# Optimization experiments

Measured on AMD Instinct MI355X. Metric: run time of the kernel, lower is better.

## Reference

```python
import jax, jax.numpy as jnp
import numpy as np

B, N, CL = 128, 64, 64


def _lin_params(key, fan_in, fan_out):
    k1, k2 = jax.random.split(key)
    bound = 1.0 / np.sqrt(fan_in)
    w = jax.random.uniform(k1, (fan_in, fan_out), jnp.float32, -bound, bound)
    b = jax.random.uniform(k2, (fan_out,), jnp.float32, -bound, bound)
    return w, b


def setup_inputs() -> dict:
    key = jax.random.key(0)
    ks = jax.random.split(key, 12)
    cl = CL
    se_w1, se_b1 = _lin_params(ks[0], cl, cl)
    se_w2, se_b2 = _lin_params(ks[1], cl, cl)
    sd_w1, sd_b1 = _lin_params(ks[2], cl, 2 * cl)
    sd_w2, sd_b2 = _lin_params(ks[3], 2 * cl, 2 * cl)
    rc_w1, rc_b1 = _lin_params(ks[4], 2 * cl + 1, 2 * cl)
    rc_w2, rc_b2 = _lin_params(ks[5], 2 * cl, 2 * cl)
    rc_w3, rc_b3 = _lin_params(ks[6], 2 * cl, 2 * cl)
    an_w1, an_b1 = _lin_params(ks[7], 2 * cl + 1, cl)
    an_w2, an_b2 = _lin_params(ks[8], cl, 2 * cl)
    s = jax.random.normal(ks[9], (B, N, cl), jnp.float32)
    return dict(s=s,
                se_w1=se_w1, se_b1=se_b1, se_w2=se_w2, se_b2=se_b2,
                sd_w1=sd_w1, sd_b1=sd_b1, sd_w2=sd_w2, sd_b2=sd_b2,
                rc_w1=rc_w1, rc_b1=rc_b1, rc_w2=rc_w2, rc_b2=rc_b2,
                rc_w3=rc_w3, rc_b3=rc_b3,
                an_w1=an_w1, an_b1=an_b1, an_w2=an_w2, an_b2=an_b2)


def reference(s, se_w1, se_b1, se_w2, se_b2,
              sd_w1, sd_b1, sd_w2, sd_b2,
              rc_w1, rc_b1, rc_w2, rc_b2, rc_w3, rc_b3,
              an_w1, an_b1, an_w2, an_b2):
    relu = jax.nn.relu
    # state encoder: [B, N, cl]
    h = relu(relu(s @ se_w1 + se_b1) @ se_w2 + se_b2)
    Bn, Nn, cl = h.shape
    # all-pairs features [B, N, N, cl]
    a1 = jnp.broadcast_to(h[:, :, None, :], (Bn, Nn, Nn, cl))  # object_arg1
    a2 = jnp.broadcast_to(h[:, None, :, :], (Bn, Nn, Nn, cl))  # object_arg2
    dist = (a1[..., 0] - a2[..., 0]) ** 2 + (a1[..., 1] - a2[..., 1]) ** 2
    feat = jnp.concatenate([a1, a2, dist[..., None]], axis=-1)  # [B,N,N,2cl+1]
    rel = relu(relu(relu(feat @ rc_w1 + rc_b1) @ rc_w2 + rc_b2) @ rc_w3 + rc_b3)
    att = jax.nn.sigmoid(relu(feat @ an_w1 + an_b1) @ an_w2 + an_b2)
    rel_dyn = jnp.mean(rel * att, axis=2)  # [B, N, 2cl]
    self_dyn = relu(h @ sd_w1 + sd_b1) @ sd_w2 + sd_b2  # [B, N, 2cl]
    return jnp.mean(self_dyn + rel_dyn, axis=1)  # [B, 2cl]
```

## Files before the change

kernel.cpp:

```cpp
#include <hip/hip_runtime.h>
#include <math.h>

#define TPB 256

typedef unsigned short u16;
typedef __attribute__((ext_vector_type(8))) short bf16x8;
typedef __attribute__((ext_vector_type(4))) float f32x4;

#define BLOB_U16 524288
#define BASE_RC_F32 327680
#define BASE_AN_F32 1376256
#define WS_NEED_BASES ((size_t)(1376256 + 524288) * 4)
#define RC1F 0
#define AN1F 16384
#define AN2F 24576
#define RC2F 40960
#define RC3F 73728

__device__ __forceinline__ float b2f(u16 h) {
  return __uint_as_float(((unsigned)h) << 16);
}
__device__ __forceinline__ void split_bf16(float x, u16& hi, u16& lo) {
  unsigned u = __float_as_uint(x);
  hi = (u16)(u >> 16);
  float hif = __uint_as_float(u & 0xFFFF0000u);
  lo = (u16)(__float_as_uint(x - hif) >> 16);
}
__device__ __forceinline__ u16 f2bf_rne(float x) {
  unsigned u = __float_as_uint(x);
  return (u16)((u + 0x7FFFu + ((u >> 16) & 1u)) >> 16);
}
__device__ __forceinline__ unsigned pack_bf16_hu(float v0, float v1) {
  unsigned a = __float_as_uint(v0) + 0x8000u;
  unsigned b = __float_as_uint(v1) + 0x8000u;
  return __builtin_amdgcn_perm(b, a, 0x07060302u);
}

__device__ __forceinline__ void cp_lds(float* dst, const float* src, int nfloats, int tid) {
  const float4* s4 = (const float4*)src;
  float4* d4 = (float4*)dst;
  const int n4 = nfloats >> 2;
  for (int i = tid; i < n4; i += TPB) d4[i] = s4[i];
}
__device__ __forceinline__ void ld4(float r[4], const float* p) {
  float4 v = *(const float4*)p;
  r[0] = v.x; r[1] = v.y; r[2] = v.z; r[3] = v.w;
}
__device__ __forceinline__ void ld2(float r[2], const float* p) {
  float2 v = *(const float2*)p;
  r[0] = v.x; r[1] = v.y;
}

__global__ __launch_bounds__(TPB, 3) void enc_prep_kernel(
    const float* __restrict__ s_in,
    const float* __restrict__ se_w1, const float* __restrict__ se_b1,
    const float* __restrict__ se_w2, const float* __restrict__ se_b2,
    const float* __restrict__ sd_w1, const float* __restrict__ sd_b1,
    const float* __restrict__ sd_w2, const float* __restrict__ sd_b2,
    const float* __restrict__ rc_w1, const float* __restrict__ rc_b1,
    const float* __restrict__ rc_w2, const float* __restrict__ rc_w3,
    const float* __restrict__ an_w1, const float* __restrict__ an_b1,
    const float* __restrict__ an_w2,
    u16* __restrict__ hB, u16* __restrict__ blob,
    float* __restrict__ baseRcG, float* __restrict__ baseAnG, int do_bases,
    float* __restrict__ out) {
  if (blockIdx.x >= 256) {
    int idx = (int)(blockIdx.x - 256) * TPB + threadIdx.x;
    if (idx >= 53248) return;
    int r, base, OK, T; const float* W; int Wld, krow0, twoTerm;
    if (idx < 8192)       { r = idx;         base = RC1F; OK = 8192;  T = 8; W = rc_w1; Wld = 128; krow0 = 64; twoTerm = 1; }
    else if (idx < 12288) { r = idx - 8192;  base = AN1F; OK = 4096;  T = 4; W = an_w1; Wld = 64;  krow0 = 64; twoTerm = 1; }
    else if (idx < 20480) { r = idx - 12288; base = AN2F; OK = 8192;  T = 8; W = an_w2; Wld = 128; krow0 = 0;  twoTerm = 0; }
    else if (idx < 36864) { r = idx - 20480; base = RC2F; OK = 16384; T = 8; W = rc_w2; Wld = 128; krow0 = 0;  twoTerm = 0; }
    else                  { r = idx - 36864; base = RC3F; OK = 16384; T = 8; W = rc_w3; Wld = 128; krow0 = 0;  twoTerm = 0; }
    const int u = r & 7;
    const int lane = (r >> 3) & 63;
    const int ct = r >> 9;
    const int c = (T == 8) ? (ct >> 3) : (ct >> 2);
    const int tg = (T == 8) ? (ct & 7) : (ct & 3);
    const int o = tg * 16 + (lane & 15);
    const int k = c * 32 + (lane >> 4) * 8 + u;
    const float x = W[(krow0 + k) * Wld + o];
    if (twoTerm) {
      u16 hi, lo; split_bf16(x, hi, lo);
      blob[base + r] = hi;
      blob[base + OK + r] = lo;
    } else {
      blob[base + r] = f2bf_rne(x);
    }
    return;
  }

  __shared__ __align__(16) float sX[2048];
  __shared__ __align__(16) float sH1[2048];
  __shared__ __align__(16) float sT[4096];
  __shared__ __align__(16) float sW[4096];
  __shared__ float sb1[64], sb2[64], sdb1[128], sdb2[128], srb1[128], sab1[64];

  const int tid = threadIdx.x;
  const int lg = tid >> 5;
  const int og = tid & 31;
  const int b = blockIdx.x >> 1;
  const int row0 = b * 64 + (blockIdx.x & 1) * 32;
  const int n0 = lg * 4;

  cp_lds(sX, s_in + row0 * 64, 2048, tid);
  cp_lds(sW, se_w1, 4096, tid);
  if (tid < 64) { sb1[tid] = se_b1[tid]; sb2[tid] = se_b2[tid]; }
  else if (tid < 192) { const int o = tid - 64; sdb1[o] = sd_b1[o]; sdb2[o] = sd_b2[o]; }
  if (tid < 128) srb1[tid] = rc_b1[tid];
  else if (tid < 192) sab1[tid - 128] = an_b1[tid - 128];
  __syncthreads();

  float a2[4][2];
#pragma unroll
  for (int nn = 0; nn < 4; nn++) { a2[nn][0] = 0.f; a2[nn][1] = 0.f; }
  for (int kk = 0; kk < 64; kk += 4) {
    float xr[4][4], wr[4][2];
#pragma unroll
    for (int nn = 0; nn < 4; nn++) ld4(xr[nn], &sX[(n0 + nn) * 64 + kk]);
#pragma unroll
    for (int t = 0; t < 4; t++) ld2(wr[t], &sW[(kk + t) * 64 + og * 2]);
#pragma unroll
    for (int t = 0; t < 4; t++)
#pragma unroll
      for (int nn = 0; nn < 4; nn++) {
        a2[nn][0] = fmaf(xr[nn][t], wr[t][0], a2[nn][0]);
        a2[nn][1] = fmaf(xr[nn][t], wr[t][1], a2[nn][1]);
      }
  }
#pragma unroll
  for (int nn = 0; nn < 4; nn++) {
    float2 v;
    v.x = fmaxf(a2[nn][0] + sb1[og * 2 + 0], 0.f);
    v.y = fmaxf(a2[nn][1] + sb1[og * 2 + 1], 0.f);
    *(float2*)&sH1[(n0 + nn) * 64 + og * 2] = v;
  }
  __syncthreads();
  cp_lds(sW, se_w2, 4096, tid);
  __syncthreads();

#pragma unroll
  for (int nn = 0; nn < 4; nn++) { a2[nn][0] = 0.f; a2[nn][1] = 0.f; }
  for (int kk = 0; kk < 64; kk += 4) {
    float xr[4][4], wr[4][2];
#pragma unroll
    for (int nn = 0; nn < 4; nn++) ld4(xr[nn], &sH1[(n0 + nn) * 64 + kk]);
#pragma unroll
    for (int t = 0; t < 4; t++) ld2(wr[t], &sW[(kk + t) * 64 + og * 2]);
#pragma unroll
    for (int t = 0; t < 4; t++)
#pragma unroll
      for (int nn = 0; nn < 4; nn++) {
        a2[nn][0] = fmaf(xr[nn][t], wr[t][0], a2[nn][0]);
        a2[nn][1] = fmaf(xr[nn][t], wr[t][1], a2[nn][1]);
      }
  }
#pragma unroll
  for (int nn = 0; nn < 4; nn++) {
    float2 v;
    v.x = fmaxf(a2[nn][0] + sb2[og * 2 + 0], 0.f);
    v.y = fmaxf(a2[nn][1] + sb2[og * 2 + 1], 0.f);
    *(float2*)&sX[(n0 + nn) * 64 + og * 2] = v;
    const int off = (row0 + n0 + nn) * 64 + og * 2;
    *(ushort2*)&hB[off] = make_ushort2(f2bf_rne(v.x), f2bf_rne(v.y));
  }
  __syncthreads();

  float a4[4][4];
#pragma unroll
  for (int nn = 0; nn < 4; nn++)
#pragma unroll
    for (int oo = 0; oo < 4; oo++) a4[nn][oo] = 0.f;
  for (int c = 0; c < 2; c++) {
    cp_lds(sW, sd_w1 + c * 32 * 128, 4096, tid);
    __syncthreads();
    for (int kk = 0; kk < 32; kk += 4) {
      float xr[4][4], wr[4][4];
#pragma unroll
      for (int nn = 0; nn < 4; nn++) ld4(xr[nn], &sX[(n0 + nn) * 64 + c * 32 + kk]);
#pragma unroll
      for (int t = 0; t < 4; t++) ld4(wr[t], &sW[(kk + t) * 128 + og * 4]);
#pragma unroll
      for (int t = 0; t < 4; t++)
#pragma unroll
        for (int nn = 0; nn < 4; nn++)
#pragma unroll
          for (int oo = 0; oo < 4; oo++)
            a4[nn][oo] = fmaf(xr[nn][t], wr[t][oo], a4[nn][oo]);
    }
    __syncthreads();
  }
#pragma unroll
  for (int nn = 0; nn < 4; nn++) {
    float4 v;
    v.x = fmaxf(a4[nn][0] + sdb1[og * 4 + 0], 0.f);
    v.y = fmaxf(a4[nn][1] + sdb1[og * 4 + 1], 0.f);
    v.z = fmaxf(a4[nn][2] + sdb1[og * 4 + 2], 0.f);
    v.w = fmaxf(a4[nn][3] + sdb1[og * 4 + 3], 0.f);
    *(float4*)&sT[(n0 + nn) * 128 + og * 4] = v;
  }
  __syncthreads();

#pragma unroll
  for (int nn = 0; nn < 4; nn++)
#pragma unroll
    for (int oo = 0; oo < 4; oo++) a4[nn][oo] = 0.f;
  for (int c = 0; c < 4; c++) {
    cp_lds(sW, sd_w2 + c * 32 * 128, 4096, tid);
    __syncthreads();
    for (int kk = 0; kk < 32; kk += 4) {
      float xr[4][4], wr[4][4];
#pragma unroll
      for (int nn = 0; nn < 4; nn++) ld4(xr[nn], &sT[(n0 + nn) * 128 + c * 32 + kk]);
#pragma unroll
      for (int t = 0; t < 4; t++) ld4(wr[t], &sW[(kk + t) * 128 + og * 4]);
#pragma unroll
      for (int t = 0; t < 4; t++)
#pragma unroll
        for (int nn = 0; nn < 4; nn++)
#pragma unroll
          for (int oo = 0; oo < 4; oo++)
            a4[nn][oo] = fmaf(xr[nn][t], wr[t][oo], a4[nn][oo]);
    }
    __syncthreads();
  }
  float p[4];
#pragma unroll
  for (int oo = 0; oo < 4; oo++)
    p[oo] = a4[0][oo] + a4[1][oo] + a4[2][oo] + a4[3][oo] + 4.f * sdb2[og * 4 + oo];
  *(float4*)&sH1[lg * 128 + og * 4] = make_float4(p[0], p[1], p[2], p[3]);
  __syncthreads();
  if (tid < 128) {
    float ssum = 0.f;
#pragma unroll
    for (int g = 0; g < 8; g++) ssum += sH1[g * 128 + tid];
    atomicAdd(&out[b * 128 + tid], ssum * (1.0f / 64.0f));
  }

  if (do_bases) {
#pragma unroll
    for (int nn = 0; nn < 4; nn++)
#pragma unroll
      for (int oo = 0; oo < 4; oo++) a4[nn][oo] = 0.f;
    for (int c = 0; c < 2; c++) {
      __syncthreads();
      cp_lds(sW, rc_w1 + c * 32 * 128, 4096, tid);
      __syncthreads();
      for (int kk = 0; kk < 32; kk += 4) {
        float xr[4][4], wr[4][4];
#pragma unroll
        for (int nn = 0; nn < 4; nn++) ld4(xr[nn], &sX[(n0 + nn) * 64 + c * 32 + kk]);
#pragma unroll
        for (int t = 0; t < 4; t++) ld4(wr[t], &sW[(kk + t) * 128 + og * 4]);
#pragma unroll
        for (int t = 0; t < 4; t++)
#pragma unroll
          for (int nn = 0; nn < 4; nn++)
#pragma unroll
            for (int oo = 0; oo < 4; oo++)
              a4[nn][oo] = fmaf(xr[nn][t], wr[t][oo], a4[nn][oo]);
      }
    }
#pragma unroll
    for (int nn = 0; nn < 4; nn++) {
      float4 v;
      v.x = a4[nn][0] + srb1[og * 4 + 0];
      v.y = a4[nn][1] + srb1[og * 4 + 1];
      v.z = a4[nn][2] + srb1[og * 4 + 2];
      v.w = a4[nn][3] + srb1[og * 4 + 3];
      *(float4*)&baseRcG[(size_t)(row0 + n0 + nn) * 128 + og * 4] = v;
    }
    __syncthreads();
    cp_lds(sW, an_w1, 4096, tid);
    __syncthreads();
#pragma unroll
    for (int nn = 0; nn < 4; nn++) { a2[nn][0] = 0.f; a2[nn][1] = 0.f; }
    for (int kk = 0; kk < 64; kk += 4) {
      float xr[4][4], wr[4][2];
#pragma unroll
      for (int nn = 0; nn < 4; nn++) ld4(xr[nn], &sX[(n0 + nn) * 64 + kk]);
#pragma unroll
      for (int t = 0; t < 4; t++) ld2(wr[t], &sW[(kk + t) * 64 + og * 2]);
#pragma unroll
      for (int t = 0; t < 4; t++)
#pragma unroll
        for (int nn = 0; nn < 4; nn++) {
          a2[nn][0] = fmaf(xr[nn][t], wr[t][0], a2[nn][0]);
          a2[nn][1] = fmaf(xr[nn][t], wr[t][1], a2[nn][1]);
        }
    }
#pragma unroll
    for (int nn = 0; nn < 4; nn++) {
      float2 v;
      v.x = a2[nn][0] + sab1[og * 2 + 0];
      v.y = a2[nn][1] + sab1[og * 2 + 1];
      *(float2*)&baseAnG[(size_t)(row0 + n0 + nn) * 64 + og * 2] = v;
    }
  }
}

template<int MT, int NCHUNK, int RSG, int TILES>
__device__ __forceinline__ void run_layer2(f32x4 (&acc)[MT][4],
    const u16* __restrict__ blobL, int OK,
    const u16* __restrict__ sB, int tg0, int quad, int l15) {
  const int lane = quad * 16 + l15;
#pragma unroll
  for (int c = 0; c < NCHUNK; ++c) {
    bf16x8 Ah[MT], Al[MT];
#pragma unroll
    for (int t = 0; t < MT; ++t) {
      const u16* p = blobL + ((c * TILES + tg0 + t) * 64 + lane) * 8;
      Ah[t] = *(const bf16x8*)p;
      Al[t] = *(const bf16x8*)(p + OK);
    }
    const int slot = (4 * c + quad) ^ (l15 & 7);
    bf16x8 Bh[4];
#pragma unroll
    for (int s = 0; s < 4; ++s)
      Bh[s] = *(const bf16x8*)&sB[(16 * s + l15) * (RSG * 8) + slot * 8];
#pragma unroll
    for (int t = 0; t < MT; ++t)
#pragma unroll
      for (int s = 0; s < 4; ++s) {
        f32x4 a = acc[t][s];
        a = __builtin_amdgcn_mfma_f32_16x16x32_bf16(Ah[t], Bh[s], a, 0, 0, 0);
        a = __builtin_amdgcn_mfma_f32_16x16x32_bf16(Al[t], Bh[s], a, 0, 0, 0);
        acc[t][s] = a;
      }
  }
}

template<int MT, int NCHUNK, int RSG, int TILES>
__device__ __forceinline__ void run_layer1(f32x4 (&acc)[MT][4],
    const u16* __restrict__ blobL,
    const u16* __restrict__ sB, int tg0, int quad, int l15) {
  const int lane = quad * 16 + l15;
#pragma unroll
  for (int c = 0; c < NCHUNK; ++c) {
    bf16x8 Ah[MT];
#pragma unroll
    for (int t = 0; t < MT; ++t)
      Ah[t] = *(const bf16x8*)(blobL + ((c * TILES + tg0 + t) * 64 + lane) * 8);
    const int slot = (4 * c + quad) ^ (l15 & 7);
    bf16x8 Bh[4];
#pragma unroll
    for (int s = 0; s < 4; ++s)
      Bh[s] = *(const bf16x8*)&sB[(16 * s + l15) * (RSG * 8) + slot * 8];
#pragma unroll
    for (int t = 0; t < MT; ++t)
#pragma unroll
      for (int s = 0; s < 4; ++s)
        acc[t][s] = __builtin_amdgcn_mfma_f32_16x16x32_bf16(Ah[t], Bh[s], acc[t][s], 0, 0, 0);
  }
}

template<int MT, int RSG>
__device__ __forceinline__ void store_acts_pk(const f32x4 (&acc)[MT][4],
                                              u16* dst, int o0, int quad, int l15) {
#pragma unroll
  for (int t = 0; t < MT; ++t) {
    const int ob = o0 + 16 * t + quad * 4;
    const int slot = (ob >> 3) ^ (l15 & 7);
    const int e = ob & 7;
#pragma unroll
    for (int s = 0; s < 4; ++s) {
      const int j = 16 * s + l15;
      uint2 pk;
      pk.x = pack_bf16_hu(fmaxf(acc[t][s][0], 0.f), fmaxf(acc[t][s][1], 0.f));
      pk.y = pack_bf16_hu(fmaxf(acc[t][s][2], 0.f), fmaxf(acc[t][s][3], 0.f));
      *(uint2*)&dst[j * (RSG * 8) + slot * 8 + e] = pk;
    }
  }
}

__global__ __launch_bounds__(TPB, 4) void pair_mfma_kernel(
    const u16* __restrict__ hB, const u16* __restrict__ blob,
    const float* __restrict__ baseRcG, const float* __restrict__ baseAnG,
    int has_bases,
    const float* __restrict__ rc_w1, const float* __restrict__ rc_b1,
    const float* __restrict__ rc_b2, const float* __restrict__ rc_b3,
    const float* __restrict__ an_w1, const float* __restrict__ an_b1,
    const float* __restrict__ an_b2,
    float* __restrict__ out) {
  __shared__ __align__(16) u16 sAct[64 * 128];
  __shared__ __align__(16) u16 sAn[64 * 64];
  __shared__ float sHi[64], sDist[64];
  __shared__ float sBaseRc[128], sBaseAn[64], sW1d[128], sAnd[64];
  __shared__ float sB2[128], sB3[128], sAb2[128], sRed[128];

  const int tid = threadIdx.x;
  const int w = tid >> 6, lane = tid & 63;
  const int quad = lane >> 4, l15 = lane & 15;
  const int b = blockIdx.x >> 6, i = blockIdx.x & 63;
  const int o0 = w * 32;
  const int o0a = w * 16;

  {
    const float4* srcJ = (const float4*)(hB + b * 4096);
    for (int idx = tid; idx < 512; idx += TPB) {
      const int row = idx >> 3, g = idx & 7;
      *(float4*)&sAct[row * 128 + ((g ^ (row & 7)) * 8)] = srcJ[idx];
    }
  }
  if (has_bases) {
    const float4* bR = (const float4*)(baseRcG + (size_t)(b * 64 + i) * 128);
    const float4* bA = (const float4*)(baseAnG + (size_t)(b * 64 + i) * 64);
    if (tid < 32) ((float4*)sBaseRc)[tid] = bR[tid];
    else if (tid < 48) ((float4*)sBaseAn)[tid - 32] = bA[tid - 32];
  }
  if (tid < 64) sHi[tid] = b2f(hB[(b * 64 + i) * 64 + tid]);
  if (tid < 128) {
    sW1d[tid] = rc_w1[128 * 128 + tid];
    sB2[tid] = rc_b2[tid]; sB3[tid] = rc_b3[tid]; sAb2[tid] = an_b2[tid];
  } else if (tid < 192) {
    sAnd[tid - 128] = an_w1[128 * 64 + (tid - 128)];
  }
  __syncthreads();
  if (!has_bases) {
    if (tid < 128) {
      float acc = rc_b1[tid];
      for (int k = 0; k < 64; ++k) acc = fmaf(sHi[k], rc_w1[k * 128 + tid], acc);
      sBaseRc[tid] = acc;
    } else if (tid < 192) {
      const int o = tid - 128;
      float acc = an_b1[o];
      for (int k = 0; k < 64; ++k) acc = fmaf(sHi[k], an_w1[k * 64 + o], acc);
      sBaseAn[o] = acc;
    }
  }
  if (tid >= 192) {
    const int j = tid - 192;
    const int base = j * 128 + ((0 ^ (j & 7)) * 8);
    const float d0 = sHi[0] - b2f(sAct[base + 0]);
    const float d1 = sHi[1] - b2f(sAct[base + 1]);
    sDist[j] = d0 * d0 + d1 * d1;
  }
  __syncthreads();

  f32x4 accR[2][4];
  f32x4 accN[1][4];
  {
    float bbR[2][4], wwR[2][4], bbN[4], wwN[4];
#pragma unroll
    for (int t = 0; t < 2; ++t) {
      ld4(bbR[t], &sBaseRc[o0 + 16 * t + quad * 4]);
      ld4(wwR[t], &sW1d[o0 + 16 * t + quad * 4]);
    }
    ld4(bbN, &sBaseAn[o0a + quad * 4]);
    ld4(wwN, &sAnd[o0a + quad * 4]);
#pragma unroll
    for (int s = 0; s < 4; ++s) {
      const float dj = sDist[16 * s + l15];
#pragma unroll
      for (int t = 0; t < 2; ++t) {
        f32x4 a;
#pragma unroll
        for (int r = 0; r < 4; ++r) a[r] = fmaf(dj, wwR[t][r], bbR[t][r]);
        accR[t][s] = a;
      }
      f32x4 a;
#pragma unroll
      for (int r = 0; r < 4; ++r) a[r] = fmaf(dj, wwN[r], bbN[r]);
      accN[0][s] = a;
    }
  }
  {
    const int lane64 = quad * 16 + l15;
#pragma unroll
    for (int c = 0; c < 2; ++c) {
      bf16x8 Ah[2], Al[2], AhN, AlN;
#pragma unroll
      for (int t = 0; t < 2; ++t) {
        const u16* p = blob + RC1F + ((c * 8 + 2 * w + t) * 64 + lane64) * 8;
        Ah[t] = *(const bf16x8*)p;
        Al[t] = *(const bf16x8*)(p + 8192);
      }
      {
        const u16* p = blob + AN1F + ((c * 4 + w) * 64 + lane64) * 8;
        AhN = *(const bf16x8*)p;
        AlN = *(const bf16x8*)(p + 4096);
      }
      const int slot = (4 * c + quad) ^ (l15 & 7);
      bf16x8 Bh[4];
#pragma unroll
      for (int s = 0; s < 4; ++s)
        Bh[s] = *(const bf16x8*)&sAct[(16 * s + l15) * 128 + slot * 8];
#pragma unroll
      for (int s = 0; s < 4; ++s) {
#pragma unroll
        for (int t = 0; t < 2; ++t) {
          f32x4 a = accR[t][s];
          a = __builtin_amdgcn_mfma_f32_16x16x32_bf16(Ah[t], Bh[s], a, 0, 0, 0);
          a = __builtin_amdgcn_mfma_f32_16x16x32_bf16(Al[t], Bh[s], a, 0, 0, 0);
          accR[t][s] = a;
        }
        f32x4 a = accN[0][s];
        a = __builtin_amdgcn_mfma_f32_16x16x32_bf16(AhN, Bh[s], a, 0, 0, 0);
        a = __builtin_amdgcn_mfma_f32_16x16x32_bf16(AlN, Bh[s], a, 0, 0, 0);
        accN[0][s] = a;
      }
    }
  }
  store_acts_pk<1, 8>(accN, sAn, o0a, quad, l15);
  __syncthreads();
  store_acts_pk<2, 16>(accR, sAct, o0, quad, l15);
  __syncthreads();

  f32x4 accT[2][4];
  {
    float bb[2][4];
#pragma unroll
    for (int t = 0; t < 2; ++t) ld4(bb[t], &sAb2[o0 + 16 * t + quad * 4]);
#pragma unroll
    for (int t = 0; t < 2; ++t)
#pragma unroll
      for (int s = 0; s < 4; ++s) {
        f32x4 a;
#pragma unroll
        for (int r = 0; r < 4; ++r) a[r] = bb[t][r];
        accT[t][s] = a;
      }
  }
  run_layer1<2, 2, 8, 8>(accT, blob + AN2F, sAn, 2 * w, quad, l15);
  float att[2][4][4];
#pragma unroll
  for (int t = 0; t < 2; ++t)
#pragma unroll
    for (int s = 0; s < 4; ++s)
#pragma unroll
      for (int r = 0; r < 4; ++r)
        att[t][s][r] = 1.0f / (1.0f + __expf(-accT[t][s][r]));

  {
    float bb[2][4];
#pragma unroll
    for (int t = 0; t < 2; ++t) ld4(bb[t], &sB2[o0 + 16 * t + quad * 4]);
#pragma unroll
    for (int t = 0; t < 2; ++t)
#pragma unroll
      for (int s = 0; s < 4; ++s) {
        f32x4 a;
#pragma unroll
        for (int r = 0; r < 4; ++r) a[r] = bb[t][r];
        accR[t][s] = a;
      }
  }
  run_layer1<2, 4, 16, 8>(accR, blob + RC2F, sAct, 2 * w, quad, l15);
  __syncthreads();
  store_acts_pk<2, 16>(accR, sAct, o0, quad, l15);
  __syncthreads();

  {
    float bb[2][4];
#pragma unroll
    for (int t = 0; t < 2; ++t) ld4(bb[t], &sB3[o0 + 16 * t + quad * 4]);
#pragma unroll
    for (int t = 0; t < 2; ++t)
#pragma unroll
      for (int s = 0; s < 4; ++s) {
        f32x4 a;
#pragma unroll
        for (int r = 0; r < 4; ++r) a[r] = bb[t][r];
        accR[t][s] = a;
      }
  }
  run_layer1<2, 4, 16, 8>(accR, blob + RC3F, sAct, 2 * w, quad, l15);
  float ps[2][4] = {{0.f, 0.f, 0.f, 0.f}, {0.f, 0.f, 0.f, 0.f}};
#pragma unroll
  for (int t = 0; t < 2; ++t)
#pragma unroll
    for (int s = 0; s < 4; ++s)
#pragma unroll
      for (int r = 0; r < 4; ++r) {
        const float rel = fmaxf(accR[t][s][r], 0.f);
        ps[t][r] = fmaf(rel, att[t][s][r], ps[t][r]);
      }
#pragma unroll
  for (int t = 0; t < 2; ++t)
#pragma unroll
    for (int r = 0; r < 4; ++r) {
      float v = ps[t][r];
      v += __shfl_xor(v, 1, 64);
      v += __shfl_xor(v, 2, 64);
      v += __shfl_xor(v, 4, 64);
      v += __shfl_xor(v, 8, 64);
      ps[t][r] = v;
    }
  if (l15 == 0) {
#pragma unroll
    for (int t = 0; t < 2; ++t)
#pragma unroll
      for (int r = 0; r < 4; ++r)
        sRed[o0 + 16 * t + quad * 4 + r] = ps[t][r];
  }
  __syncthreads();
  if (tid < 128)
    atomicAdd(&out[b * 128 + tid], sRed[tid] * (1.0f / 4096.0f));
}

extern "C" void kernel_launch(void* const* d_in, const int* in_sizes, int n_in,
                              void* d_out, int out_size, void* d_ws, size_t ws_size,
                              hipStream_t stream) {
  const float* s     = (const float*)d_in[0];
  const float* se_w1 = (const float*)d_in[1];
  const float* se_b1 = (const float*)d_in[2];
  const float* se_w2 = (const float*)d_in[3];
  const float* se_b2 = (const float*)d_in[4];
  const float* sd_w1 = (const float*)d_in[5];
  const float* sd_b1 = (const float*)d_in[6];
  const float* sd_w2 = (const float*)d_in[7];
  const float* sd_b2 = (const float*)d_in[8];
  const float* rc_w1 = (const float*)d_in[9];
  const float* rc_b1 = (const float*)d_in[10];
  const float* rc_w2 = (const float*)d_in[11];
  const float* rc_b2 = (const float*)d_in[12];
  const float* rc_w3 = (const float*)d_in[13];
  const float* rc_b3 = (const float*)d_in[14];
  const float* an_w1 = (const float*)d_in[15];
  const float* an_b1 = (const float*)d_in[16];
  const float* an_w2 = (const float*)d_in[17];
  const float* an_b2 = (const float*)d_in[18];
  float* out = (float*)d_out;
  u16* hB   = (u16*)d_ws;
  u16* blob = hB + BLOB_U16;
  float* baseRcG = (float*)d_ws + BASE_RC_F32;
  float* baseAnG = (float*)d_ws + BASE_AN_F32;
  const int do_bases = (ws_size >= WS_NEED_BASES) ? 1 : 0;
  (void)n_in; (void)in_sizes;

  hipMemsetAsync(d_out, 0, (size_t)out_size * sizeof(float), stream);
  enc_prep_kernel<<<464, TPB, 0, stream>>>(s, se_w1, se_b1, se_w2, se_b2,
                                           sd_w1, sd_b1, sd_w2, sd_b2,
                                           rc_w1, rc_b1, rc_w2, rc_w3,
                                           an_w1, an_b1, an_w2,
                                           hB, blob, baseRcG, baseAnG, do_bases, out);
  pair_mfma_kernel<<<8192, TPB, 0, stream>>>(hB, blob, baseRcG, baseAnG, do_bases,
                                             rc_w1, rc_b1, rc_b2, rc_b3,
                                             an_w1, an_b1, an_b2, out);
}
```

Measured before the change: 213.0 us.

## Precompute the per-j half of the first pair layers in the encoder kernel

Result: slower. 222.8 us (+4.6%).

```diff
diff --git a/kernel.cpp b/kernel.cpp
--- a/kernel.cpp
+++ b/kernel.cpp
@@ -10,7 +10,10 @@
 #define BLOB_U16 524288
 #define BASE_RC_F32 327680
 #define BASE_AN_F32 1376256
-#define WS_NEED_BASES ((size_t)(1376256 + 524288) * 4)
+#define RC1P_F32 1900544
+#define AN1P_F32 2949120
+#define WS_NEED_BASES ((size_t)1900544 * 4)
+#define WS_NEED_PRE   ((size_t)3473408 * 4)
 #define RC1F 0
 #define AN1F 16384
 #define AN2F 24576
@@ -62,7 +65,9 @@
     const float* __restrict__ an_w1, const float* __restrict__ an_b1,
     const float* __restrict__ an_w2,
     u16* __restrict__ hB, u16* __restrict__ blob,
-    float* __restrict__ baseRcG, float* __restrict__ baseAnG, int do_bases,
+    float* __restrict__ baseRcG, float* __restrict__ baseAnG,
+    float* __restrict__ rc1pG, float* __restrict__ an1pG,
+    int do_bases, int do_pre,
     float* __restrict__ out) {
   if (blockIdx.x >= 256) {
     int idx = (int)(blockIdx.x - 256) * TPB + threadIdx.x;
@@ -101,7 +106,8 @@
   const int lg = tid >> 5;
   const int og = tid & 31;
   const int b = blockIdx.x >> 1;
-  const int row0 = b * 64 + (blockIdx.x & 1) * 32;
+  const int half = blockIdx.x & 1;
+  const int row0 = b * 64 + half * 32;
   const int n0 = lg * 4;
 
   cp_lds(sX, s_in + row0 * 64, 2048, tid);
@@ -298,36 +304,64 @@
       *(float2*)&baseAnG[(size_t)(row0 + n0 + nn) * 64 + og * 2] = v;
     }
   }
-}
-
-template<int MT, int NCHUNK, int RSG, int TILES>
-__device__ __forceinline__ void run_layer2(f32x4 (&acc)[MT][4],
-    const u16* __restrict__ blobL, int OK,
-    const u16* __restrict__ sB, int tg0, int quad, int l15) {
-  const int lane = quad * 16 + l15;
-#pragma unroll
-  for (int c = 0; c < NCHUNK; ++c) {
-    bf16x8 Ah[MT], Al[MT];
-#pragma unroll
-    for (int t = 0; t < MT; ++t) {
-      const u16* p = blobL + ((c * TILES + tg0 + t) * 64 + lane) * 8;
-      Ah[t] = *(const bf16x8*)p;
-      Al[t] = *(const bf16x8*)(p + OK);
-    }
-    const int slot = (4 * c + quad) ^ (l15 & 7);
-    bf16x8 Bh[4];
-#pragma unroll
-    for (int s = 0; s < 4; ++s)
-      Bh[s] = *(const bf16x8*)&sB[(16 * s + l15) * (RSG * 8) + slot * 8];
-#pragma unroll
-    for (int t = 0; t < MT; ++t)
-#pragma unroll
-      for (int s = 0; s < 4; ++s) {
-        f32x4 a = acc[t][s];
-        a = __builtin_amdgcn_mfma_f32_16x16x32_bf16(Ah[t], Bh[s], a, 0, 0, 0);
-        a = __builtin_amdgcn_mfma_f32_16x16x32_bf16(Al[t], Bh[s], a, 0, 0, 0);
-        acc[t][s] = a;
-      }
+
+  if (do_pre) {
+#pragma unroll
+    for (int nn = 0; nn < 4; nn++)
+#pragma unroll
+      for (int oo = 0; oo < 4; oo++) a4[nn][oo] = 0.f;
+    for (int c = 0; c < 2; c++) {
+      __syncthreads();
+      cp_lds(sW, rc_w1 + (64 + c * 32) * 128, 4096, tid);
+      __syncthreads();
+      for (int kk = 0; kk < 32; kk += 4) {
+        float xr[4][4], wr[4][4];
+#pragma unroll
+        for (int nn = 0; nn < 4; nn++) ld4(xr[nn], &sX[(n0 + nn) * 64 + c * 32 + kk]);
+#pragma unroll
+        for (int t = 0; t < 4; t++) ld4(wr[t], &sW[(kk + t) * 128 + og * 4]);
+#pragma unroll
+        for (int t = 0; t < 4; t++)
+#pragma unroll
+          for (int nn = 0; nn < 4; nn++)
+#pragma unroll
+            for (int oo = 0; oo < 4; oo++)
+              a4[nn][oo] = fmaf(xr[nn][t], wr[t][oo], a4[nn][oo]);
+      }
+    }
+#pragma unroll
+    for (int nn = 0; nn < 4; nn++) {
+      const int jl = half * 32 + n0 + nn;
+      const int addr = ((b * 8 + (og >> 2)) * 4 + (jl >> 4)) * 256 +
+                       ((og & 3) * 16 + (jl & 15)) * 4;
+      *(float4*)&rc1pG[addr] = make_float4(a4[nn][0], a4[nn][1], a4[nn][2], a4[nn][3]);
+    }
+    __syncthreads();
+    cp_lds(sW, an_w1 + 64 * 64, 4096, tid);
+    __syncthreads();
+#pragma unroll
+    for (int nn = 0; nn < 4; nn++) { a2[nn][0] = 0.f; a2[nn][1] = 0.f; }
+    for (int kk = 0; kk < 64; kk += 4) {
+      float xr[4][4], wr[4][2];
+#pragma unroll
+      for (int nn = 0; nn < 4; nn++) ld4(xr[nn], &sX[(n0 + nn) * 64 + kk]);
+#pragma unroll
+      for (int t = 0; t < 4; t++) ld2(wr[t], &sW[(kk + t) * 64 + og * 2]);
+#pragma unroll
+      for (int t = 0; t < 4; t++)
+#pragma unroll
+        for (int nn = 0; nn < 4; nn++) {
+          a2[nn][0] = fmaf(xr[nn][t], wr[t][0], a2[nn][0]);
+          a2[nn][1] = fmaf(xr[nn][t], wr[t][1], a2[nn][1]);
+        }
+    }
+#pragma unroll
+    for (int nn = 0; nn < 4; nn++) {
+      const int jl = half * 32 + n0 + nn;
+      const int addr = ((b * 4 + (og >> 3)) * 4 + (jl >> 4)) * 256 +
+                       (((og >> 1) & 3) * 16 + (jl & 15)) * 4 + (og & 1) * 2;
+      *(float2*)&an1pG[addr] = make_float2(a2[nn][0], a2[nn][1]);
+    }
   }
 }
 
@@ -374,10 +408,11 @@
   }
 }
 
-__global__ __launch_bounds__(TPB, 4) void pair_mfma_kernel(
+__global__ __launch_bounds__(TPB, 5) void pair_mfma_kernel(
     const u16* __restrict__ hB, const u16* __restrict__ blob,
     const float* __restrict__ baseRcG, const float* __restrict__ baseAnG,
-    int has_bases,
+    const float* __restrict__ rc1pG, const float* __restrict__ an1pG,
+    int has_bases, int has_pre,
     const float* __restrict__ rc_w1, const float* __restrict__ rc_b1,
     const float* __restrict__ rc_b2, const float* __restrict__ rc_b3,
     const float* __restrict__ an_w1, const float* __restrict__ an_b1,
@@ -396,51 +431,29 @@
   const int o0 = w * 32;
   const int o0a = w * 16;
 
-  {
-    const float4* srcJ = (const float4*)(hB + b * 4096);
-    for (int idx = tid; idx < 512; idx += TPB) {
-      const int row = idx >> 3, g = idx & 7;
-      *(float4*)&sAct[row * 128 + ((g ^ (row & 7)) * 8)] = srcJ[idx];
-    }
-  }
-  if (has_bases) {
-    const float4* bR = (const float4*)(baseRcG + (size_t)(b * 64 + i) * 128);
-    const float4* bA = (const float4*)(baseAnG + (size_t)(b * 64 + i) * 64);
-    if (tid < 32) ((float4*)sBaseRc)[tid] = bR[tid];
-    else if (tid < 48) ((float4*)sBaseAn)[tid - 32] = bA[tid - 32];
-  }
-  if (tid < 64) sHi[tid] = b2f(hB[(b * 64 + i) * 64 + tid]);
-  if (tid < 128) {
-    sW1d[tid] = rc_w1[128 * 128 + tid];
-    sB2[tid] = rc_b2[tid]; sB3[tid] = rc_b3[tid]; sAb2[tid] = an_b2[tid];
-  } else if (tid < 192) {
-    sAnd[tid - 128] = an_w1[128 * 64 + (tid - 128)];
-  }
-  __syncthreads();
-  if (!has_bases) {
-    if (tid < 128) {
-      float acc = rc_b1[tid];
-      for (int k = 0; k < 64; ++k) acc = fmaf(sHi[k], rc_w1[k * 128 + tid], acc);
-      sBaseRc[tid] = acc;
-    } else if (tid < 192) {
-      const int o = tid - 128;
-      float acc = an_b1[o];
-      for (int k = 0; k < 64; ++k) acc = fmaf(sHi[k], an_w1[k * 64 + o], acc);
-      sBaseAn[o] = acc;
-    }
-  }
-  if (tid >= 192) {
-    const int j = tid - 192;
-    const int base = j * 128 + ((0 ^ (j & 7)) * 8);
-    const float d0 = sHi[0] - b2f(sAct[base + 0]);
-    const float d1 = sHi[1] - b2f(sAct[base + 1]);
-    sDist[j] = d0 * d0 + d1 * d1;
-  }
-  __syncthreads();
-
   f32x4 accR[2][4];
   f32x4 accN[1][4];
-  {
+
+  if (has_pre) {
+    if (tid < 128) {
+      sW1d[tid] = rc_w1[128 * 128 + tid];
+      sB2[tid] = rc_b2[tid]; sB3[tid] = rc_b3[tid]; sAb2[tid] = an_b2[tid];
+    } else if (tid < 192) {
+      sAnd[tid - 128] = an_w1[128 * 64 + (tid - 128)];
+    } else {
+      const int j = tid - 192;
+      const float hi0 = b2f(hB[(b * 64 + i) * 64 + 0]);
+      const float hi1 = b2f(hB[(b * 64 + i) * 64 + 1]);
+      const ushort2 hj = *(const ushort2*)&hB[(b * 64 + j) * 64];
+      const float d0 = hi0 - b2f(hj.x), d1 = hi1 - b2f(hj.y);
+      sDist[j] = d0 * d0 + d1 * d1;
+    }
+    if (tid < 32)
+      ((float4*)sBaseRc)[tid] = ((const float4*)(baseRcG + (size_t)(b * 64 + i) * 128))[tid];
+    else if (tid < 48)
+      ((float4*)sBaseAn)[tid - 32] = ((const float4*)(baseAnG + (size_t)(b * 64 + i) * 64))[tid - 32];
+    __syncthreads();
+
     float bbR[2][4], wwR[2][4], bbN[4], wwN[4];
 #pragma unroll
     for (int t = 0; t < 2; ++t) {
@@ -449,63 +462,142 @@
     }
     ld4(bbN, &sBaseAn[o0a + quad * 4]);
     ld4(wwN, &sAnd[o0a + quad * 4]);
+    const float* pR = rc1pG + (size_t)(b * 8 + 2 * w) * 1024 + lane * 4;
+    const float* pA = an1pG + (size_t)(b * 4 + w) * 1024 + lane * 4;
 #pragma unroll
     for (int s = 0; s < 4; ++s) {
       const float dj = sDist[16 * s + l15];
 #pragma unroll
       for (int t = 0; t < 2; ++t) {
+        const float4 pre = *(const float4*)(pR + t * 1024 + s * 256);
         f32x4 a;
-#pragma unroll
-        for (int r = 0; r < 4; ++r) a[r] = fmaf(dj, wwR[t][r], bbR[t][r]);
+        a[0] = pre.x + fmaf(dj, wwR[t][0], bbR[t][0]);
+        a[1] = pre.y + fmaf(dj, wwR[t][1], bbR[t][1]);
+        a[2] = pre.z + fmaf(dj, wwR[t][2], bbR[t][2]);
+        a[3] = pre.w + fmaf(dj, wwR[t][3], bbR[t][3]);
         accR[t][s] = a;
       }
+      const float4 pre = *(const float4*)(pA + s * 256);
       f32x4 a;
-#pragma unroll
-      for (int r = 0; r < 4; ++r) a[r] = fmaf(dj, wwN[r], bbN[r]);
+      a[0] = pre.x + fmaf(dj, wwN[0], bbN[0]);
+      a[1] = pre.y + fmaf(dj, wwN[1], bbN[1]);
+      a[2] = pre.z + fmaf(dj, wwN[2], bbN[2]);
+      a[3] = pre.w + fmaf(dj, wwN[3], bbN[3]);
       accN[0][s] = a;
     }
-  }
-  {
-    const int lane64 = quad * 16 + l15;
-#pragma unroll
-    for (int c = 0; c < 2; ++c) {
-      bf16x8 Ah[2], Al[2], AhN, AlN;
+    store_acts_pk<1, 8>(accN, sAn, o0a, quad, l15);
+    store_acts_pk<2, 16>(accR, sAct, o0, quad, l15);
+    __syncthreads();
+  } else {
+    {
+      const float4* srcJ = (const float4*)(hB + b * 4096);
+      for (int idx = tid; idx < 512; idx += TPB) {
+        const int row = idx >> 3, g = idx & 7;
+        *(float4*)&sAct[row * 128 + ((g ^ (row & 7)) * 8)] = srcJ[idx];
+      }
+    }
+    if (has_bases) {
+      const float4* bR = (const float4*)(baseRcG + (size_t)(b * 64 + i) * 128);
+      const float4* bA = (const float4*)(baseAnG + (size_t)(b * 64 + i) * 64);
+      if (tid < 32) ((float4*)sBaseRc)[tid] = bR[tid];
+      else if (tid < 48) ((float4*)sBaseAn)[tid - 32] = bA[tid - 32];
+    }
+    if (tid < 64) sHi[tid] = b2f(hB[(b * 64 + i) * 64 + tid]);
+    if (tid < 128) {
+      sW1d[tid] = rc_w1[128 * 128 + tid];
+      sB2[tid] = rc_b2[tid]; sB3[tid] = rc_b3[tid]; sAb2[tid] = an_b2[tid];
+    } else if (tid < 192) {
+      sAnd[tid - 128] = an_w1[128 * 64 + (tid - 128)];
+    }
+    __syncthreads();
+    if (!has_bases) {
+      if (tid < 128) {
+        float acc = rc_b1[tid];
+        for (int k = 0; k < 64; ++k) acc = fmaf(sHi[k], rc_w1[k * 128 + tid], acc);
+        sBaseRc[tid] = acc;
+      } else if (tid < 192) {
+        const int o = tid - 128;
+        float acc = an_b1[o];
+        for (int k = 0; k < 64; ++k) acc = fmaf(sHi[k], an_w1[k * 64 + o], acc);
+        sBaseAn[o] = acc;
+      }
+    }
+    if (tid >= 192) {
+      const int j = tid - 192;
+      const int base = j * 128 + ((0 ^ (j & 7)) * 8);
+      const float d0 = sHi[0] - b2f(sAct[base + 0]);
+      const float d1 = sHi[1] - b2f(sAct[base + 1]);
+      sDist[j] = d0 * d0 + d1 * d1;
+    }
+    __syncthreads();
+
+    {
+      float bbR[2][4], wwR[2][4], bbN[4], wwN[4];
 #pragma unroll
       for (int t = 0; t < 2; ++t) {
-        const u16* p = blob + RC1F + ((c * 8 + 2 * w + t) * 64 + lane64) * 8;
-        Ah[t] = *(const bf16x8*)p;
-        Al[t] = *(const bf16x8*)(p + 8192);
-      }
-      {
-        const u16* p = blob + AN1F + ((c * 4 + w) * 64 + lane64) * 8;
-        AhN = *(const bf16x8*)p;
-        AlN = *(const bf16x8*)(p + 4096);
-      }
-      const int slot = (4 * c + quad) ^ (l15 & 7);
-      bf16x8 Bh[4];
-#pragma unroll
-      for (int s = 0; s < 4; ++s)
-        Bh[s] = *(const bf16x8*)&sAct[(16 * s + l15) * 128 + slot * 8];
+        ld4(bbR[t], &sBaseRc[o0 + 16 * t + quad * 4]);
+        ld4(wwR[t], &sW1d[o0 + 16 * t + quad * 4]);
+      }
+      ld4(bbN, &sBaseAn[o0a + quad * 4]);
+      ld4(wwN, &sAnd[o0a + quad * 4]);
 #pragma unroll
       for (int s = 0; s < 4; ++s) {
+        const float dj = sDist[16 * s + l15];
 #pragma unroll
         for (int t = 0; t < 2; ++t) {
-          f32x4 a = accR[t][s];
-          a = __builtin_amdgcn_mfma_f32_16x16x32_bf16(Ah[t], Bh[s], a, 0, 0, 0);
-          a = __builtin_amdgcn_mfma_f32_16x16x32_bf16(Al[t], Bh[s], a, 0, 0, 0);
+          f32x4 a;
+#pragma unroll
+          for (int r = 0; r < 4; ++r) a[r] = fmaf(dj, wwR[t][r], bbR[t][r]);
           accR[t][s] = a;
         }
-        f32x4 a = accN[0][s];
-        a = __builtin_amdgcn_mfma_f32_16x16x32_bf16(AhN, Bh[s], a, 0, 0, 0);
-        a = __builtin_amdgcn_mfma_f32_16x16x32_bf16(AlN, Bh[s], a, 0, 0, 0);
+        f32x4 a;
+#pragma unroll
+        for (int r = 0; r < 4; ++r) a[r] = fmaf(dj, wwN[r], bbN[r]);
         accN[0][s] = a;
       }
     }
-  }
-  store_acts_pk<1, 8>(accN, sAn, o0a, quad, l15);
-  __syncthreads();
-  store_acts_pk<2, 16>(accR, sAct, o0, quad, l15);
-  __syncthreads();
+    {
+      const int lane64 = quad * 16 + l15;
+#pragma unroll
+      for (int c = 0; c < 2; ++c) {
+        bf16x8 Ah[2], Al[2], AhN, AlN;
+#pragma unroll
+        for (int t = 0; t < 2; ++t) {
+          const u16* p = blob + RC1F + ((c * 8 + 2 * w + t) * 64 + lane64) * 8;
+          Ah[t] = *(const bf16x8*)p;
+          Al[t] = *(const bf16x8*)(p + 8192);
+        }
+        {
+          const u16* p = blob + AN1F + ((c * 4 + w) * 64 + lane64) * 8;
+          AhN = *(const bf16x8*)p;
+          AlN = *(const bf16x8*)(p + 4096);
+        }
+        const int slot = (4 * c + quad) ^ (l15 & 7);
+        bf16x8 Bh[4];
+#pragma unroll
+        for (int s = 0; s < 4; ++s)
+          Bh[s] = *(const bf16x8*)&sAct[(16 * s + l15) * 128 + slot * 8];
+#pragma unroll
+        for (int s = 0; s < 4; ++s) {
+#pragma unroll
+          for (int t = 0; t < 2; ++t) {
+            f32x4 a = accR[t][s];
+            a = __builtin_amdgcn_mfma_f32_16x16x32_bf16(Ah[t], Bh[s], a, 0, 0, 0);
+            a = __builtin_amdgcn_mfma_f32_16x16x32_bf16(Al[t], Bh[s], a, 0, 0, 0);
+            accR[t][s] = a;
+          }
+          f32x4 a = accN[0][s];
+          a = __builtin_amdgcn_mfma_f32_16x16x32_bf16(AhN, Bh[s], a, 0, 0, 0);
+          a = __builtin_amdgcn_mfma_f32_16x16x32_bf16(AlN, Bh[s], a, 0, 0, 0);
+          accN[0][s] = a;
+        }
+      }
+    }
+    store_acts_pk<1, 8>(accN, sAn, o0a, quad, l15);
+    __syncthreads();
+    store_acts_pk<2, 16>(accR, sAct, o0, quad, l15);
+    __syncthreads();
+  }
 
   f32x4 accT[2][4];
   {
@@ -626,7 +718,10 @@
   u16* blob = hB + BLOB_U16;
   float* baseRcG = (float*)d_ws + BASE_RC_F32;
   float* baseAnG = (float*)d_ws + BASE_AN_F32;
-  const int do_bases = (ws_size >= WS_NEED_BASES) ? 1 : 0;
+  float* rc1pG   = (float*)d_ws + RC1P_F32;
+  float* an1pG   = (float*)d_ws + AN1P_F32;
+  const int has_pre   = (ws_size >= WS_NEED_PRE) ? 1 : 0;
+  const int has_bases = (ws_size >= WS_NEED_BASES) ? 1 : 0;
   (void)n_in; (void)in_sizes;
 
   hipMemsetAsync(d_out, 0, (size_t)out_size * sizeof(float), stream);
@@ -634,8 +729,10 @@
                                            sd_w1, sd_b1, sd_w2, sd_b2,
                                            rc_w1, rc_b1, rc_w2, rc_w3,
                                            an_w1, an_b1, an_w2,
-                                           hB, blob, baseRcG, baseAnG, do_bases, out);
-  pair_mfma_kernel<<<8192, TPB, 0, stream>>>(hB, blob, baseRcG, baseAnG, do_bases,
+                                           hB, blob, baseRcG, baseAnG, rc1pG, an1pG,
+                                           has_bases, has_pre, out);
+  pair_mfma_kernel<<<8192, TPB, 0, stream>>>(hB, blob, baseRcG, baseAnG, rc1pG, an1pG,
+                                             has_bases, has_pre,
                                              rc_w1, rc_b1, rc_b2, rc_b3,
                                              an_w1, an_b1, an_b2, out);
 }
```
